# Optimization experiments

Hardware: AMD Instinct MI355X
Metric: run time of the kernel (lower is better)

The kernel has to match this reference:

```python
import jax, jax.numpy as jnp
import numpy as np

B, S, D = 8, 2048, 512
FF = 2048
E = 8

def setup_inputs() -> dict:
    key = jax.random.key(0)
    ks = jax.random.split(key, 7)
    s = 1.0 / np.sqrt(D)
    sf = 1.0 / np.sqrt(FF)
    return {
        "x":  jax.random.normal(ks[0], (B, S, D), dtype=jnp.float32),
        "Wg": jax.random.uniform(ks[1], (D, E), jnp.float32, -s, s),
        "bg": jax.random.uniform(ks[2], (E,), jnp.float32, -s, s),
        "W1": jax.random.uniform(ks[3], (E, D, FF), jnp.float32, -s, s),
        "b1": jax.random.uniform(ks[4], (E, FF), jnp.float32, -s, s),
        "W2": jax.random.uniform(ks[5], (E, FF, D), jnp.float32, -sf, sf),
        "b2": jax.random.uniform(ks[6], (E, D), jnp.float32, -sf, sf),
    }

def reference(x, Wg, bg, W1, b1, W2, b2):
    b, s, d = x.shape
    xf = x.reshape(-1, d)                      # [T, D]
    logits = xf @ Wg + bg                      # [T, E]
    probs = jax.nn.softmax(logits, axis=-1)
    pmax = jnp.max(probs, axis=-1)             # [T]
    routes = jnp.argmax(probs, axis=-1)        # [T] int
    xs = xf * pmax[:, None]                    # scale tokens by router prob
    # per-expert FFN over all tokens, select the routed expert's output
    out_tok = jnp.zeros_like(xf)
    for e in range(E):
        h = jax.nn.relu(xs @ W1[e] + b1[e])    # [T, FF]
        y = h @ W2[e] + b2[e]                  # [T, D]
        out_tok = jnp.where((routes == e)[:, None], y, out_tok)
    # torch.cat of per-expert nonzero-index gathers == tokens stably sorted by expert id
    order = jnp.argsort(routes)                # jnp.argsort is stable
    return out_tok[order].reshape(b, s, d)
```

## Files before the change

kernel.cpp:

```cpp
#include <hip/hip_runtime.h>
#include <hip/hip_bf16.h>

constexpr int TTOK  = 16384;
constexpr int DDIM  = 512;
constexpr int FFDIM = 2048;
constexpr int NEXP  = 8;
constexpr int GB_TOK = 16;
constexpr int NGB    = TTOK / GB_TOK;
constexpr int MAXTILES = TTOK / 128 + NEXP;

typedef __attribute__((ext_vector_type(8))) short short8_t;
typedef __attribute__((ext_vector_type(4))) float f32x4_t;

__device__ __forceinline__ unsigned short f2bf(float f) {
    union { float f; unsigned u; } v; v.f = f;
    return (unsigned short)((v.u + 0x7fffu + ((v.u >> 16) & 1u)) >> 16);
}

__device__ __forceinline__ void gl_lds16(const void* g, void* l) {
    __builtin_amdgcn_global_load_lds(
        (const __attribute__((address_space(1))) void*)g,
        (__attribute__((address_space(3))) void*)l,
        16, 0, 0);
}

__global__ __launch_bounds__(256) void transpose_cvt2(const float* __restrict__ W1,
                                                      const float* __restrict__ W2,
                                                      unsigned short* __restrict__ W1T,
                                                      unsigned short* __restrict__ W2T) {
    __shared__ float tile[32][33];
    int z = blockIdx.z;
    bool isW2 = z >= NEXP;
    int e = isW2 ? z - NEXP : z;
    int R = isW2 ? FFDIM : DDIM;
    int C = isW2 ? DDIM : FFDIM;
    int tilesC = C / 32;
    int t = blockIdx.x;
    int c0 = (t % tilesC) * 32;
    int r0 = (t / tilesC) * 32;
    const float* s = (isW2 ? W2 : W1) + (size_t)e * DDIM * FFDIM;
    unsigned short* d = (isW2 ? W2T : W1T) + (size_t)e * DDIM * FFDIM;
    int tx = threadIdx.x & 31, ty = threadIdx.x >> 5;
    #pragma unroll
    for (int i = 0; i < 4; i++)
        tile[ty + 8 * i][tx] = s[(size_t)(r0 + ty + 8 * i) * C + c0 + tx];
    __syncthreads();
    #pragma unroll
    for (int i = 0; i < 4; i++)
        d[(size_t)(c0 + ty + 8 * i) * R + r0 + tx] = f2bf(tile[tx][ty + 8 * i]);
}

__global__ __launch_bounds__(256) void gate_kernel(const float* __restrict__ x,
                                                   const float* __restrict__ Wg,
                                                   const float* __restrict__ bg,
                                                   int* __restrict__ route,
                                                   float* __restrict__ pmax,
                                                   int* __restrict__ blockCounts) {
    __shared__ int cnt[NEXP];
    __shared__ float bgs[NEXP];
    int tid = threadIdx.x;
    if (tid < NEXP) { cnt[tid] = 0; bgs[tid] = bg[tid]; }
    __syncthreads();
    int wave = tid >> 6, lane = tid & 63;
    float w[8][8];
    #pragma unroll
    for (int jj = 0; jj < 8; jj++) {
        float4 a = *(const float4*)(Wg + (size_t)(lane * 8 + jj) * NEXP);
        float4 b = *(const float4*)(Wg + (size_t)(lane * 8 + jj) * NEXP + 4);
        w[jj][0] = a.x; w[jj][1] = a.y; w[jj][2] = a.z; w[jj][3] = a.w;
        w[jj][4] = b.x; w[jj][5] = b.y; w[jj][6] = b.z; w[jj][7] = b.w;
    }
    int tbase = blockIdx.x * GB_TOK + wave * 4;
    for (int it = 0; it < 4; it++) {
        int t = tbase + it;
        float4 xa = *(const float4*)(x + (size_t)t * DDIM + lane * 8);
        float4 xb = *(const float4*)(x + (size_t)t * DDIM + lane * 8 + 4);
        float xs[8] = {xa.x, xa.y, xa.z, xa.w, xb.x, xb.y, xb.z, xb.w};
        double acc[NEXP];
        #pragma unroll
        for (int e = 0; e < NEXP; e++) acc[e] = 0.0;
        #pragma unroll
        for (int jj = 0; jj < 8; jj++) {
            double xv = (double)xs[jj];
            #pragma unroll
            for (int e = 0; e < NEXP; e++) acc[e] += xv * (double)w[jj][e];
        }
        #pragma unroll
        for (int off = 32; off > 0; off >>= 1) {
            #pragma unroll
            for (int e = 0; e < NEXP; e++) acc[e] += __shfl_down(acc[e], off);
        }
        if (lane == 0) {
            double l[NEXP];
            #pragma unroll
            for (int e = 0; e < NEXP; e++) l[e] = acc[e] + (double)bgs[e];
            int r = 0; double lm = l[0];
            #pragma unroll
            for (int e = 1; e < NEXP; e++) if (l[e] > lm) { lm = l[e]; r = e; }
            double s = 0.0;
            #pragma unroll
            for (int e = 0; e < NEXP; e++) s += exp(l[e] - lm);
            route[t] = r;
            pmax[t] = (float)(1.0 / s);
            atomicAdd(&cnt[r], 1);
        }
    }
    __syncthreads();
    if (tid < NEXP) blockCounts[blockIdx.x * NEXP + tid] = cnt[tid];
}

__global__ __launch_bounds__(1024) void scan_kernel(const int* __restrict__ blockCounts,
                                                    int* __restrict__ blockOffsets,
                                                    int* __restrict__ segPrefix,
                                                    int* __restrict__ tilePrefix) {
    __shared__ int sc[NGB][NEXP];
    __shared__ int base[NEXP + 1];
    int b = threadIdx.x;
    int c[NEXP];
    #pragma unroll
    for (int e = 0; e < NEXP; e++) { c[e] = blockCounts[b * NEXP + e]; sc[b][e] = c[e]; }
    __syncthreads();
    for (int off = 1; off < NGB; off <<= 1) {
        int t[NEXP];
        if (b >= off) {
            #pragma unroll
            for (int e = 0; e < NEXP; e++) t[e] = sc[b - off][e];
        }
        __syncthreads();
        if (b >= off) {
            #pragma unroll
            for (int e = 0; e < NEXP; e++) sc[b][e] += t[e];
        }
        __syncthreads();
    }
    if (b == 0) {
        int s = 0;
        #pragma unroll
        for (int e = 0; e < NEXP; e++) { base[e] = s; s += sc[NGB - 1][e]; }
        base[NEXP] = s;
        for (int e = 0; e <= NEXP; e++) segPrefix[e] = base[e];
        int tp = 0;
        tilePrefix[0] = 0;
        for (int e = 0; e < NEXP; e++) {
            tp += (sc[NGB - 1][e] + 127) / 128;
            tilePrefix[e + 1] = tp;
        }
    }
    __syncthreads();
    #pragma unroll
    for (int e = 0; e < NEXP; e++)
        blockOffsets[b * NEXP + e] = base[e] + sc[b][e] - c[e];
}

__global__ __launch_bounds__(256) void scatter_kernel(const float* __restrict__ x,
                                                      const int* __restrict__ route,
                                                      const float* __restrict__ pmax,
                                                      const int* __restrict__ blockOffsets,
                                                      unsigned short* __restrict__ Xs) {
    __shared__ int dstL[GB_TOK];
    __shared__ float pmL[GB_TOK];
    int tid = threadIdx.x;
    int bb = blockIdx.x;
    if (tid < GB_TOK) {
        int t = bb * GB_TOK + tid;
        int r = route[t];
        unsigned long long ltmask = (tid == 0) ? 0ull : ((~0ull) >> (64 - tid));
        int rank = 0;
        #pragma unroll
        for (int e = 0; e < NEXP; e++) {
            unsigned long long m = __ballot(r == e);
            if (r == e) rank = __popcll(m & ltmask);
        }
        dstL[tid] = blockOffsets[bb * NEXP + r] + rank;
        pmL[tid] = pmax[t];
    }
    __syncthreads();
    int wave = tid >> 6, lane = tid & 63;
    for (int rr = 0; rr < 4; rr++) {
        int rowl = wave * 4 + rr;
        int t = bb * GB_TOK + rowl;
        float pm = pmL[rowl];
        const float4* xr = (const float4*)(x + (size_t)t * DDIM) + lane * 2;
        float4 a = xr[0], b = xr[1];
        union { short8_t v; unsigned short s[8]; } o;
        o.s[0] = f2bf(a.x * pm); o.s[1] = f2bf(a.y * pm);
        o.s[2] = f2bf(a.z * pm); o.s[3] = f2bf(a.w * pm);
        o.s[4] = f2bf(b.x * pm); o.s[5] = f2bf(b.y * pm);
        o.s[6] = f2bf(b.z * pm); o.s[7] = f2bf(b.w * pm);
        *(short8_t*)(Xs + (size_t)dstL[rowl] * DDIM + lane * 8) = o.v;
    }
}

template <bool RELU, typename OutT>
__global__ __launch_bounds__(256) void gemm_seg(const unsigned short* __restrict__ A,
                                                const unsigned short* __restrict__ Bt,
                                                const float* __restrict__ bias,
                                                OutT* __restrict__ C,
                                                const int* __restrict__ segPrefix,
                                                const int* __restrict__ tilePrefix,
                                                int K, int N) {
    int t = blockIdx.x;
    if (t >= tilePrefix[NEXP]) return;
    int e = 0;
    #pragma unroll
    for (int i = 1; i <= NEXP; i++) e += (t >= tilePrefix[i]) ? 1 : 0;
    int seg1 = segPrefix[e + 1];
    int m0 = segPrefix[e] + (t - tilePrefix[e]) * 128;
    int n0 = blockIdx.y * 128;

    __shared__ unsigned short As[2 * 4096];
    __shared__ unsigned short Bs[2 * 4096];

    int tid = threadIdx.x, wave = tid >> 6, lane = tid & 63;
    const unsigned short* Bte = Bt + (size_t)e * N * K;

    int srow = lane >> 2;
    int sg   = (lane & 3) ^ ((lane >> 2) & 3) ^ ((lane >> 4) & 3);
    int scol = sg * 8;

    f32x4_t acc[4][4];
    #pragma unroll
    for (int i = 0; i < 4; i++)
        #pragma unroll
        for (int j = 0; j < 4; j++) acc[i][j] = (f32x4_t){0.f, 0.f, 0.f, 0.f};

    int wm = (wave & 1) * 64;
    int wn = (wave >> 1) * 64;
    int frow = lane & 15;
    int gr = lane >> 4;
    int fswz = (gr ^ (frow & 3) ^ ((frow >> 2) & 3)) * 8;

    for (int kc = 0; kc < K; kc += 64) {
        #pragma unroll
        for (int p = 0; p < 2; p++) {
            #pragma unroll
            for (int i = 0; i < 2; i++) {
                int reg = wave * 2 + i;
                int arow = m0 + reg * 16 + srow;
                arow = arow < TTOK ? arow : TTOK - 1;
                gl_lds16(A + (size_t)arow * K + kc + p * 32 + scol, &As[p * 4096 + reg * 512]);
                int brow = n0 + reg * 16 + srow;
                gl_lds16(Bte + (size_t)brow * K + kc + p * 32 + scol, &Bs[p * 4096 + reg * 512]);
            }
        }
        __syncthreads();
        #pragma unroll
        for (int p = 0; p < 2; p++) {
            short8_t af[4], bfr[4];
            #pragma unroll
            for (int i = 0; i < 4; i++)
                af[i] = *(const short8_t*)&As[p * 4096 + (wm + i * 16 + frow) * 32 + fswz];
            #pragma unroll
            for (int j = 0; j < 4; j++)
                bfr[j] = *(const short8_t*)&Bs[p * 4096 + (wn + j * 16 + frow) * 32 + fswz];
            #pragma unroll
            for (int i = 0; i < 4; i++)
                #pragma unroll
                for (int j = 0; j < 4; j++)
                    acc[i][j] = __builtin_amdgcn_mfma_f32_16x16x32_bf16(af[i], bfr[j], acc[i][j], 0, 0, 0);
        }
        __syncthreads();
    }

    int quad = lane >> 4;
    int colb = lane & 15;
    float bv[4];
    #pragma unroll
    for (int j = 0; j < 4; j++) bv[j] = bias[(size_t)e * N + n0 + wn + j * 16 + colb];

    if constexpr (sizeof(OutT) == 2) {
        unsigned short* cbuf = As;
        #pragma unroll
        for (int p = 0; p < 2; p++) {
            __syncthreads();
            if ((wave >> 1) == p) {
                #pragma unroll
                for (int i = 0; i < 4; i++)
                    #pragma unroll
                    for (int j = 0; j < 4; j++)
                        #pragma unroll
                        for (int r = 0; r < 4; r++) {
                            float v = acc[i][j][r] + bv[j];
                            if (RELU) v = fmaxf(v, 0.0f);
                            cbuf[(wm + i * 16 + quad * 4 + r) * 72 + j * 16 + colb] = f2bf(v);
                        }
            }
            __syncthreads();
            int row = tid >> 1, ch = (tid & 1) * 32;
            int grow = m0 + row;
            if (grow < seg1) {
                #pragma unroll
                for (int k = 0; k < 4; k++) {
                    short8_t v = *(const short8_t*)&cbuf[row * 72 + ch + k * 8];
                    *(short8_t*)&C[(size_t)grow * N + n0 + p * 64 + ch + k * 8] = v;
                }
            }
        }
    } else {
        #pragma unroll
        for (int i = 0; i < 4; i++) {
            #pragma unroll
            for (int j = 0; j < 4; j++) {
                int col = n0 + wn + j * 16 + colb;
                #pragma unroll
                for (int r = 0; r < 4; r++) {
                    int row = m0 + wm + i * 16 + quad * 4 + r;
                    if (row < seg1) {
                        float v = acc[i][j][r] + bv[j];
                        if (RELU) v = fmaxf(v, 0.0f);
                        C[(size_t)row * N + col] = v;
                    }
                }
            }
        }
    }
}

extern "C" void kernel_launch(void* const* d_in, const int* in_sizes, int n_in,
                              void* d_out, int out_size, void* d_ws, size_t ws_size,
                              hipStream_t stream) {
    const float* x  = (const float*)d_in[0];
    const float* Wg = (const float*)d_in[1];
    const float* bg = (const float*)d_in[2];
    const float* W1 = (const float*)d_in[3];
    const float* b1 = (const float*)d_in[4];
    const float* W2 = (const float*)d_in[5];
    const float* b2 = (const float*)d_in[6];
    float* out = (float*)d_out;

    char* ws = (char*)d_ws;
    size_t off = 0;
    auto alloc = [&](size_t bytes) -> char* {
        char* p = ws + off;
        off += (bytes + 255) & ~(size_t)255;
        return p;
    };
    unsigned short* W1T = (unsigned short*)alloc((size_t)NEXP * DDIM * FFDIM * 2);
    unsigned short* W2T = (unsigned short*)alloc((size_t)NEXP * DDIM * FFDIM * 2);
    unsigned short* Xs  = (unsigned short*)alloc((size_t)TTOK * DDIM * 2);
    unsigned short* H   = (unsigned short*)alloc((size_t)TTOK * FFDIM * 2);
    int*   route        = (int*)alloc((size_t)TTOK * 4);
    float* pmaxArr      = (float*)alloc((size_t)TTOK * 4);
    int*   blockCounts  = (int*)alloc((size_t)NGB * NEXP * 4);
    int*   blockOffsets = (int*)alloc((size_t)NGB * NEXP * 4);
    int*   segPrefix    = (int*)alloc((size_t)(NEXP + 1) * 4);
    int*   tilePrefix   = (int*)alloc((size_t)(NEXP + 1) * 4);

    transpose_cvt2<<<dim3(1024, 1, 2 * NEXP), 256, 0, stream>>>(W1, W2, W1T, W2T);
    gate_kernel<<<NGB, 256, 0, stream>>>(x, Wg, bg, route, pmaxArr, blockCounts);
    scan_kernel<<<1, NGB, 0, stream>>>(blockCounts, blockOffsets, segPrefix, tilePrefix);
    scatter_kernel<<<NGB, 256, 0, stream>>>(x, route, pmaxArr, blockOffsets, Xs);
    gemm_seg<true, unsigned short><<<dim3(MAXTILES, FFDIM / 128, 1), 256, 0, stream>>>(
        Xs, W1T, b1, H, segPrefix, tilePrefix, DDIM, FFDIM);
    gemm_seg<false, float><<<dim3(MAXTILES, DDIM / 128, 1), 256, 0, stream>>>(
        H, W2T, b2, out, segPrefix, tilePrefix, FFDIM, DDIM);
}
```

Baseline: 313.4 us.

## Fuse scan into gate kernel via last-block pattern and widen weight transpose tiles

Removes the separate scan kernel: each gate block publishes its expert counts, and the last block to finish (detected with an atomic counter) performs the prefix scan over all block counts and writes the offsets and prefixes. The weight transpose/convert kernel moves to 64x64 tiles with float4 loads and 16-byte bf16 stores, and runs after scatter. This cuts one launch plus a serialized single-block kernel and makes the transpose traffic more coalesced. In exchange it adds a memset launch and threadfence-based cross-block synchronization.

```diff
diff --git a/kernel.cpp b/kernel.cpp
--- a/kernel.cpp
+++ b/kernel.cpp
@@ -28,26 +28,39 @@
                                                       const float* __restrict__ W2,
                                                       unsigned short* __restrict__ W1T,
                                                       unsigned short* __restrict__ W2T) {
-    __shared__ float tile[32][33];
-    int z = blockIdx.z;
+    __shared__ float lds[64 * 65];
+    int z = blockIdx.y;
     bool isW2 = z >= NEXP;
     int e = isW2 ? z - NEXP : z;
     int R = isW2 ? FFDIM : DDIM;
     int C = isW2 ? DDIM : FFDIM;
-    int tilesC = C / 32;
+    int tilesC = C / 64;
     int t = blockIdx.x;
-    int c0 = (t % tilesC) * 32;
-    int r0 = (t / tilesC) * 32;
+    int c0 = (t % tilesC) * 64;
+    int r0 = (t / tilesC) * 64;
     const float* s = (isW2 ? W2 : W1) + (size_t)e * DDIM * FFDIM;
     unsigned short* d = (isW2 ? W2T : W1T) + (size_t)e * DDIM * FFDIM;
-    int tx = threadIdx.x & 31, ty = threadIdx.x >> 5;
-    #pragma unroll
-    for (int i = 0; i < 4; i++)
-        tile[ty + 8 * i][tx] = s[(size_t)(r0 + ty + 8 * i) * C + c0 + tx];
-    __syncthreads();
-    #pragma unroll
-    for (int i = 0; i < 4; i++)
-        d[(size_t)(c0 + ty + 8 * i) * R + r0 + tx] = f2bf(tile[tx][ty + 8 * i]);
+    int tid = threadIdx.x;
+    int lr = tid >> 4, lc = (tid & 15) * 4;
+    #pragma unroll
+    for (int p = 0; p < 4; p++) {
+        int r = p * 16 + lr;
+        float4 v = *(const float4*)(s + (size_t)(r0 + r) * C + c0 + lc);
+        lds[r * 65 + lc]     = v.x;
+        lds[r * 65 + lc + 1] = v.y;
+        lds[r * 65 + lc + 2] = v.z;
+        lds[r * 65 + lc + 3] = v.w;
+    }
+    __syncthreads();
+    int rr = (tid & 7) * 8, cbase = tid >> 3;
+    #pragma unroll
+    for (int p = 0; p < 2; p++) {
+        int cc = p * 32 + cbase;
+        union { short8_t v; unsigned short u[8]; } o;
+        #pragma unroll
+        for (int k = 0; k < 8; k++) o.u[k] = f2bf(lds[(rr + k) * 65 + cc]);
+        *(short8_t*)(d + (size_t)(c0 + cc) * R + r0 + rr) = o.v;
+    }
 }
 
 __global__ __launch_bounds__(256) void gate_kernel(const float* __restrict__ x,
@@ -55,9 +68,15 @@
                                                    const float* __restrict__ bg,
                                                    int* __restrict__ route,
                                                    float* __restrict__ pmax,
-                                                   int* __restrict__ blockCounts) {
+                                                   int* __restrict__ blockCounts,
+                                                   int* __restrict__ blockOffsets,
+                                                   int* __restrict__ segPrefix,
+                                                   int* __restrict__ tilePrefix,
+                                                   int* __restrict__ doneCtr) {
     __shared__ int cnt[NEXP];
     __shared__ float bgs[NEXP];
+    __shared__ int sc2[256][NEXP];
+    __shared__ int winner;
     int tid = threadIdx.x;
     if (tid < NEXP) { cnt[tid] = 0; bgs[tid] = bg[tid]; }
     __syncthreads();
@@ -106,50 +125,64 @@
         }
     }
     __syncthreads();
-    if (tid < NEXP) blockCounts[blockIdx.x * NEXP + tid] = cnt[tid];
-}
-
-__global__ __launch_bounds__(1024) void scan_kernel(const int* __restrict__ blockCounts,
-                                                    int* __restrict__ blockOffsets,
-                                                    int* __restrict__ segPrefix,
-                                                    int* __restrict__ tilePrefix) {
-    __shared__ int sc[NGB][NEXP];
-    __shared__ int base[NEXP + 1];
-    int b = threadIdx.x;
-    int c[NEXP];
-    #pragma unroll
-    for (int e = 0; e < NEXP; e++) { c[e] = blockCounts[b * NEXP + e]; sc[b][e] = c[e]; }
-    __syncthreads();
-    for (int off = 1; off < NGB; off <<= 1) {
-        int t[NEXP];
-        if (b >= off) {
-            #pragma unroll
-            for (int e = 0; e < NEXP; e++) t[e] = sc[b - off][e];
+    if (tid == 0) {
+        #pragma unroll
+        for (int e = 0; e < NEXP; e++) blockCounts[blockIdx.x * NEXP + e] = cnt[e];
+        __threadfence();
+        winner = (atomicAdd(doneCtr, 1) == NGB - 1) ? 1 : 0;
+    }
+    __syncthreads();
+    if (!winner) return;
+    __threadfence();
+
+    int tt[NEXP];
+    #pragma unroll
+    for (int e = 0; e < NEXP; e++) tt[e] = 0;
+    #pragma unroll
+    for (int j = 0; j < 4; j++)
+        #pragma unroll
+        for (int e = 0; e < NEXP; e++) tt[e] += blockCounts[(tid * 4 + j) * NEXP + e];
+    #pragma unroll
+    for (int e = 0; e < NEXP; e++) sc2[tid][e] = tt[e];
+    __syncthreads();
+    for (int off = 1; off < 256; off <<= 1) {
+        int tv[NEXP];
+        bool valid = tid >= off;
+        if (valid) {
+            #pragma unroll
+            for (int e = 0; e < NEXP; e++) tv[e] = sc2[tid - off][e];
         }
         __syncthreads();
-        if (b >= off) {
-            #pragma unroll
-            for (int e = 0; e < NEXP; e++) sc[b][e] += t[e];
+        if (valid) {
+            #pragma unroll
+            for (int e = 0; e < NEXP; e++) sc2[tid][e] += tv[e];
         }
         __syncthreads();
     }
-    if (b == 0) {
-        int s = 0;
-        #pragma unroll
-        for (int e = 0; e < NEXP; e++) { base[e] = s; s += sc[NGB - 1][e]; }
-        base[NEXP] = s;
-        for (int e = 0; e <= NEXP; e++) segPrefix[e] = base[e];
+    int segb[NEXP + 1];
+    segb[0] = 0;
+    #pragma unroll
+    for (int e = 0; e < NEXP; e++) segb[e + 1] = segb[e] + sc2[255][e];
+    if (tid == 0) {
+        for (int e = 0; e <= NEXP; e++) segPrefix[e] = segb[e];
         int tp = 0;
         tilePrefix[0] = 0;
         for (int e = 0; e < NEXP; e++) {
-            tp += (sc[NGB - 1][e] + 127) / 128;
+            tp += (sc2[255][e] + 127) / 128;
             tilePrefix[e + 1] = tp;
         }
     }
-    __syncthreads();
-    #pragma unroll
-    for (int e = 0; e < NEXP; e++)
-        blockOffsets[b * NEXP + e] = base[e] + sc[b][e] - c[e];
+    int run[NEXP];
+    #pragma unroll
+    for (int e = 0; e < NEXP; e++) run[e] = segb[e] + sc2[tid][e] - tt[e];
+    #pragma unroll
+    for (int j = 0; j < 4; j++)
+        #pragma unroll
+        for (int e = 0; e < NEXP; e++) {
+            int v = blockCounts[(tid * 4 + j) * NEXP + e];
+            blockOffsets[(tid * 4 + j) * NEXP + e] = run[e];
+            run[e] += v;
+        }
 }
 
 __global__ __launch_bounds__(256) void scatter_kernel(const float* __restrict__ x,
@@ -345,11 +378,13 @@
     int*   blockOffsets = (int*)alloc((size_t)NGB * NEXP * 4);
     int*   segPrefix    = (int*)alloc((size_t)(NEXP + 1) * 4);
     int*   tilePrefix   = (int*)alloc((size_t)(NEXP + 1) * 4);
-
-    transpose_cvt2<<<dim3(1024, 1, 2 * NEXP), 256, 0, stream>>>(W1, W2, W1T, W2T);
-    gate_kernel<<<NGB, 256, 0, stream>>>(x, Wg, bg, route, pmaxArr, blockCounts);
-    scan_kernel<<<1, NGB, 0, stream>>>(blockCounts, blockOffsets, segPrefix, tilePrefix);
+    int*   doneCtr      = (int*)alloc(256);
+
+    hipMemsetAsync(doneCtr, 0, 4, stream);
+    gate_kernel<<<NGB, 256, 0, stream>>>(x, Wg, bg, route, pmaxArr, blockCounts,
+                                         blockOffsets, segPrefix, tilePrefix, doneCtr);
     scatter_kernel<<<NGB, 256, 0, stream>>>(x, route, pmaxArr, blockOffsets, Xs);
+    transpose_cvt2<<<dim3(256, 2 * NEXP), 256, 0, stream>>>(W1, W2, W1T, W2T);
     gemm_seg<true, unsigned short><<<dim3(MAXTILES, FFDIM / 128, 1), 256, 0, stream>>>(
         Xs, W1T, b1, H, segPrefix, tilePrefix, DDIM, FFDIM);
     gemm_seg<false, float><<<dim3(MAXTILES, DDIM / 128, 1), 256, 0, stream>>>(
```

New measurement: 341.0 us. 1.09x slower.
